# Optimization experiments

Hardware: AMD Instinct MI355X
Metric: run time of the kernel (lower is better)

## Reference

```python
import jax, jax.numpy as jnp
import numpy as np

OBS = jnp.array([0, 3, 6, 9, 12])
LO, HI = 0.001, 2.0

def gamma(x):
    return LO + (HI - LO) * jax.nn.sigmoid(x)

def full_chain_rhs(y, k):
    # y: (B,13) species, k: (B,19) rate constants
    A, B_, C, D, E, F, G, H, I, J, K_, L, M = [y[..., i] for i in range(13)]
    (kf1, kf2, kf3, kf4, kf5, kf6, kf7, kf8, kf9, kf10, kf11, kf12,
     kr1, kr3, kr5, kr7, kr9, kr11, kr12) = [k[..., i] for i in range(19)]
    dA = -kf1 * A + kr1 * B_
    dB = kf1 * A - kr1 * B_ - kf2 * B_
    dC = kf2 * B_ - kf3 * C + kr3 * D
    dD = kf3 * C - kr3 * D - kf4 * D
    dE = kf4 * D - kf5 * E + kr5 * F
    dF = kf5 * E - kr5 * F - kf6 * F
    dG = kf6 * F - kf7 * G + kr7 * H
    dH = kf7 * G - kr7 * H - kf8 * H
    dI = kf8 * H - kf9 * I + kr9 * J
    dJ = kf9 * I - kr9 * J - kf10 * J
    dK = kf10 * J - kf11 * K_ + kr11 * L
    dL = kf11 * K_ - kr11 * L - kf12 * L + kr12 * M
    dM = kf12 * L - kr12 * M
    return jnp.stack([dA, dB, dC, dD, dE, dF, dG, dH, dI, dJ, dK, dL, dM], axis=-1)

def rk4_step(y, dt, k):
    # y:(B,13) dt:(B,1) k:(B,19)
    k1 = full_chain_rhs(y, k)
    k2 = full_chain_rhs(y + 0.5 * dt * k1, k)
    k3 = full_chain_rhs(y + 0.5 * dt * k2, k)
    k4 = full_chain_rhs(y + dt * k3, k)
    return jnp.maximum(y + dt / 6.0 * (k1 + 2.0 * k2 + 2.0 * k3 + k4), 0.0)

def setup_inputs() -> dict:
    B, K, U, P = 2048, 256, 4, 5
    LIFT, HID = 32, 128
    key = jax.random.key(0)
    ks = jax.random.split(key, 9)
    in_dim = U + P
    def xavier(k, shape):
        lim = np.sqrt(6.0 / (shape[0] + shape[1])).astype(np.float32)
        return jax.random.uniform(k, shape, jnp.float32, -lim, lim)
    return {
        "y0": jax.random.uniform(ks[0], (B, P), jnp.float32),
        "u_seq": jax.random.normal(ks[1], (B, K, U), jnp.float32) * 0.1,
        "dt_seq": jax.random.uniform(ks[2], (B, K), jnp.float32, 0.01, 0.1),
        "y_seq": jax.random.uniform(ks[3], (B, K, P), jnp.float32),
        "W_lift": xavier(ks[4], (in_dim, LIFT)),
        "b_lift": jnp.zeros((LIFT,), jnp.float32),
        "w_ih": xavier(ks[5], (3 * HID, LIFT)),
        "w_hh": xavier(ks[6], (3 * HID, HID)),
        "b_ih": jnp.zeros((3 * HID,), jnp.float32),
        "b_hh": jnp.zeros((3 * HID,), jnp.float32),
        "W_head": xavier(ks[7], (HID, 19)),
        "b_head": jnp.zeros((19,), jnp.float32),
        "u_to_y_jump": jax.random.normal(ks[8], (U, P), jnp.float32) * 0.05,
        "tf_every": 50,
    }

def reference(y0, u_seq, dt_seq, y_seq, W_lift, b_lift, w_ih, w_hh, b_ih, b_hh, W_head, b_head, u_to_y_jump, tf_every):
    B, K, _ = u_seq.shape
    HID = w_hh.shape[1]
    # init hidden full state: 0.01 everywhere, obs slots get y0 + 0.01
    y_full0 = jnp.full((B, 13), 0.01, u_seq.dtype).at[:, OBS].set(y0 + 0.01)
    h0 = jnp.zeros((B, HID), u_seq.dtype)
    t = jnp.arange(K)
    tf_mask = (t > 0) & (t % tf_every == 0)  # teacher-forcing steps
    y_seq_prev = jnp.concatenate([jnp.zeros_like(y_seq[:, :1]), y_seq[:, :-1]], axis=1)
    xs = (jnp.swapaxes(u_seq, 0, 1), dt_seq.T[..., None],
          jnp.swapaxes(y_seq_prev, 0, 1), tf_mask)

    def step(carry, x):
        y_full, h = carry
        u_k, dt_k, y_prev_tf, m = x
        y_obs_prev = y_full[:, OBS]
        y_prev_in = jax.lax.stop_gradient(jnp.where(m, y_prev_tf, y_obs_prev))
        feat = jnp.concatenate([u_k, y_prev_in], axis=-1)
        lifted = jax.nn.silu(feat @ W_lift + b_lift)
        # PyTorch GRU cell
        gx = lifted @ w_ih.T + b_ih
        gh = h @ w_hh.T + b_hh
        rx, zx, nx = jnp.split(gx, 3, axis=-1)
        rh, zh, nh = jnp.split(gh, 3, axis=-1)
        r = jax.nn.sigmoid(rx + rh)
        z = jax.nn.sigmoid(zx + zh)
        n = jnp.tanh(nx + r * nh)
        h_new = (1.0 - z) * n + z * h
        theta = gamma(h_new @ W_head + b_head)  # (B,19), all bounds (0.001,2.0)
        y_obs_jump = y_obs_prev + u_k @ u_to_y_jump
        y_full_jump = y_full.at[:, OBS].set(y_obs_jump)
        y_full_next = rk4_step(y_full_jump, dt_k, theta)  # n_sub=1 as in forward
        return (y_full_next, h_new), (y_full_next[:, OBS], theta)

    _, (y_out, theta_out) = jax.lax.scan(step, (y_full0, h0), xs)
    return jnp.swapaxes(y_out, 0, 1), jnp.swapaxes(theta_out, 0, 1)
```

## Files before the change

### kernel.cpp

```cpp
#include <hip/hip_runtime.h>
#include <cstddef>
#include <cstdint>

#define NB 8
#define NTHREADS 640
#define HID 128
#define LIFT 32
#define NSP 13
#define NTH 19

typedef __attribute__((ext_vector_type(8))) short short8;
typedef __attribute__((ext_vector_type(4))) float f32x4;

__device__ const int c_kA [13] = {19,0,1,2,3,4,5,6,7,8,9,10,11};
__device__ const int c_kB1[13] = {0,12,2,13,4,14,6,15,8,16,10,17,18};
__device__ const int c_kB2[13] = {19,1,19,3,19,5,19,7,19,9,19,11,19};
__device__ const int c_kC [13] = {12,19,13,19,14,19,15,19,16,19,17,18,19};

__device__ __forceinline__ uint32_t pk(float a, float b) {
  uint32_t ua = __float_as_uint(a), ub = __float_as_uint(b);
  ua = (ua + 0x7FFFu + ((ua >> 16) & 1u)) >> 16;
  ub = (ub + 0x7FFFu + ((ub >> 16) & 1u)) >> 16;
  return ua | (ub << 16);
}
__device__ __forceinline__ float sigm(float a) { return 1.f/(1.f + __expf(-a)); }

__device__ __forceinline__ void sync_lds() {
  __builtin_amdgcn_sched_barrier(0);
  asm volatile("s_waitcnt lgkmcnt(0)" ::: "memory");
  __builtin_amdgcn_s_barrier();
  __builtin_amdgcn_sched_barrier(0);
}

__device__ __forceinline__ float rhs3(int am1, int ap1, float cA, float cB,
                                      float cC, float yc) {
  const float ym1 = __int_as_float(__builtin_amdgcn_ds_bpermute(am1, __float_as_int(yc)));
  const float yp1 = __int_as_float(__builtin_amdgcn_ds_bpermute(ap1, __float_as_int(yc)));
  return fmaf(cA, ym1, fmaf(cB, yc, cC * yp1));
}

union FragU { uint4 u; short8 s; };
__device__ __forceinline__ short8 ldfrag(const float* p) {
  FragU t;
  const float4 a = *reinterpret_cast<const float4*>(p);
  const float4 b = *reinterpret_cast<const float4*>(p+4);
  t.u = make_uint4(pk(a.x,a.y), pk(a.z,a.w), pk(b.x,b.y), pk(b.z,b.w));
  return t.s;
}

struct Smem {
  uint32_t whF[8*3*4*64*4];
  uint32_t whdF[2*4*64*4];
  uint32_t hF[4*64*4];
  uint32_t liftF[64*4];
  float theta[8*20];
};

__global__ __launch_bounds__(NTHREADS)
void fullmodel_rnn(const float* __restrict__ y0,
                   const float* __restrict__ u_seq,
                   const float* __restrict__ dt_seq,
                   const float* __restrict__ y_seq,
                   const float* __restrict__ W_lift,
                   const float* __restrict__ b_lift,
                   const float* __restrict__ w_ih,
                   const float* __restrict__ w_hh,
                   const float* __restrict__ b_ih,
                   const float* __restrict__ b_hh,
                   const float* __restrict__ W_head,
                   const float* __restrict__ b_head,
                   const float* __restrict__ u2y,
                   const int*  __restrict__ tf_every_p,
                   float* __restrict__ out,
                   int K, int theta_off)
{
  extern __shared__ __align__(16) char smem_raw[];
  Smem& S = *reinterpret_cast<Smem*>(smem_raw);

  const int tid  = threadIdx.x;
  const int wid  = tid >> 6;
  const int lane = tid & 63;
  const int q    = lane >> 4;
  const int col  = lane & 15;
  const int bg0  = blockIdx.x * NB;
  const int tf_every = tf_every_p[0];
  const bool gatew = (wid < 8);

  for (int f = tid; f < 8*3*4*64; f += NTHREADS) {
    int l = f & 63, idx = f >> 6;
    int s = idx & 3; idx >>= 2;
    int g = idx % 3, w = idx / 3;
    int row = 128*g + 16*w + (l & 15);
    int k0 = 32*s + 8*(l >> 4);
    const float* p = w_hh + (size_t)row*HID + k0;
    uint32_t* d = S.whF + (size_t)f*4;
    d[0]=pk(p[0],p[1]); d[1]=pk(p[2],p[3]); d[2]=pk(p[4],p[5]); d[3]=pk(p[6],p[7]);
  }
  for (int f = tid; f < 2*4*64; f += NTHREADS) {
    int l = f & 63, idx = f >> 6;
    int s = idx & 3, T = idx >> 2;
    int o = 16*T + (l & 15);
    int k0 = 32*s + 8*(l >> 4);
    uint32_t* d = S.whdF + (size_t)f*4;
    if (o < NTH) {
#pragma unroll
      for (int c=0;c<4;++c)
        d[c] = pk(W_head[(size_t)(k0+2*c)*NTH + o], W_head[(size_t)(k0+2*c+1)*NTH + o]);
    } else {
#pragma unroll
      for (int c=0;c<4;++c) d[c] = 0u;
    }
  }
  for (int f = tid; f < 4*64*4; f += NTHREADS) S.hF[f] = 0u;
  for (int f = tid; f < 64*4;   f += NTHREADS) S.liftF[f] = 0u;
  if (tid < 8) S.theta[tid*20 + 19] = 0.f;

  const uint32_t* hf_p  = &S.hF[lane*4];
  const uint32_t* lf_p  = &S.liftF[lane*4];
  const uint32_t* whp   = S.whF + ((size_t)wid*12*64 + lane)*4;
  const uint32_t* whdp  = S.whdF + (size_t)lane*4;

  float bsumR[4], bsumZ[4], bihn_[4], bhhn_[4], h_old[4];
  short8 wir, wiz, win;
  if (gatew) {
    const int rowR = 16*wid + col, kq = 8*q;
    wir = ldfrag(w_ih + (size_t)rowR*LIFT + kq);
    wiz = ldfrag(w_ih + (size_t)(128+rowR)*LIFT + kq);
    win = ldfrag(w_ih + (size_t)(256+rowR)*LIFT + kq);
#pragma unroll
    for (int r2=0;r2<4;++r2) {
      const int i0 = 16*wid + 4*q + r2;
      bsumR[r2] = b_ih[i0]     + b_hh[i0];
      bsumZ[r2] = b_ih[128+i0] + b_hh[128+i0];
      bihn_[r2] = b_ih[256+i0];
      bhhn_[r2] = b_hh[256+i0];
      h_old[r2] = 0.f;
    }
  }

  float bhd[2][4] = {{0,0,0,0},{0,0,0,0}};
  float wa0=0,wa1=0,wa2=0,wa3=0,wa4=0,wa5=0,wa6=0,wa7=0,wa8=0;
  float wb0=0,wb1=0,wb2=0,wb3=0,wb4=0,wb5=0,wb6=0,wb7=0,wb8=0;
  float blA=0.f, blB=0.f;
  const int base_b = (wid == 9) ? 4 : 0;
  const int b_loc = lane / NSP, rs = lane - NSP*b_loc;
  const bool rk_lane = (!gatew) && (lane < 52);
  const int bl8 = base_b + b_loc;
  const int gb = bg0 + (rk_lane ? bl8 : 0);
  const int gbL = bg0 + base_b + (lane >> 4);
  const bool obs = rk_lane && (rs % 3 == 0);
  const int ro = rs / 3;
  float y_reg=0.f, f_src=0.f;
  float u2yv[4]={0,0,0,0};
  int kA_=0,kB1_=0,kB2_=0,kC_=0;
  int am1=0, ap1=0, tfc=1;
  float dt_c=0.f, ysq_c=0.f;
  float4 ujc = {0,0,0,0};
  float* outT0 = out; float* outY = out;
  if (!gatew) {
#pragma unroll
    for (int T=0;T<2;++T)
#pragma unroll
      for (int r2=0;r2<4;++r2) {
        const int o = 16*T + 4*q + r2;
        bhd[T][r2] = (o < NTH) ? b_head[o] : 0.f;
      }
    const int li = 2*col;
    wa0=W_lift[0*32+li]; wa1=W_lift[1*32+li]; wa2=W_lift[2*32+li];
    wa3=W_lift[3*32+li]; wa4=W_lift[4*32+li]; wa5=W_lift[5*32+li];
    wa6=W_lift[6*32+li]; wa7=W_lift[7*32+li]; wa8=W_lift[8*32+li];
    wb0=W_lift[0*32+li+1]; wb1=W_lift[1*32+li+1]; wb2=W_lift[2*32+li+1];
    wb3=W_lift[3*32+li+1]; wb4=W_lift[4*32+li+1]; wb5=W_lift[5*32+li+1];
    wb6=W_lift[6*32+li+1]; wb7=W_lift[7*32+li+1]; wb8=W_lift[8*32+li+1];
    blA = b_lift[li]; blB = b_lift[li+1];
    outT0 = out + (size_t)theta_off + ((size_t)(bg0+col))*K*NTH + 4*q;
    __builtin_amdgcn_s_setprio(2);
  }
  if (rk_lane) {
    kA_ = c_kA[rs]; kB1_ = c_kB1[rs]; kB2_ = c_kB2[rs]; kC_ = c_kC[rs];
    am1 = 4 * ((lane > 0)  ? (lane - 1) : 0);
    ap1 = 4 * ((lane < 51) ? (lane + 1) : 51);
    y_reg = 0.01f + (obs ? y0[gb*5 + ro] : 0.f);
    if (obs) { for (int d=0;d<4;++d) u2yv[d] = u2y[d*5 + ro]; }
    f_src = y_reg;
    outY = out + ((size_t)gb*K)*5 + ro;
  }
  sync_lds();

  for (int k = 0; k <= K; ++k) {
    f32x4 accR={0,0,0,0}, accZ={0,0,0,0}, accNH={0,0,0,0};

    if (gatew) {
      if (k < K) {
        FragU h0,h1,h2,h3;
        h0.u = *reinterpret_cast<const uint4*>(hf_p);
        h1.u = *reinterpret_cast<const uint4*>(hf_p + 256);
        h2.u = *reinterpret_cast<const uint4*>(hf_p + 512);
        h3.u = *reinterpret_cast<const uint4*>(hf_p + 768);
#pragma unroll
        for (int ss=0; ss<4; ++ss) {
          FragU ar,az,an;
          ar.u = *reinterpret_cast<const uint4*>(whp + (0*4+ss)*256);
          az.u = *reinterpret_cast<const uint4*>(whp + (1*4+ss)*256);
          an.u = *reinterpret_cast<const uint4*>(whp + (2*4+ss)*256);
          const short8 hb = (ss==0)?h0.s:(ss==1)?h1.s:(ss==2)?h2.s:h3.s;
          accR  = __builtin_amdgcn_mfma_f32_16x16x32_bf16(ar.s, hb, accR, 0,0,0);
          accZ  = __builtin_amdgcn_mfma_f32_16x16x32_bf16(az.s, hb, accZ, 0,0,0);
          accNH = __builtin_amdgcn_mfma_f32_16x16x32_bf16(an.s, hb, accNH, 0,0,0);
        }
      }
    } else {
      float dt_p=0.f, ysq_p=0.f;
      float4 ujp = {0,0,0,0}, ul = {0,0,0,0};
      if (k < K) {
        if (rk_lane) {
          dt_p = dt_seq[(size_t)gb*K + k];
          ujp  = *reinterpret_cast<const float4*>(u_seq + ((size_t)gb*K + k)*4);
          if (obs) ysq_p = y_seq[((size_t)gb*K + k)*5 + ro];
        }
        ul = *reinterpret_cast<const float4*>(u_seq + ((size_t)gbL*K + k)*4);
      }
      if (k >= 1) {
        f32x4 at0={0,0,0,0}, at1={0,0,0,0};
        FragU h0,h1,h2,h3;
        h0.u = *reinterpret_cast<const uint4*>(hf_p);
        h1.u = *reinterpret_cast<const uint4*>(hf_p + 256);
        h2.u = *reinterpret_cast<const uint4*>(hf_p + 512);
        h3.u = *reinterpret_cast<const uint4*>(hf_p + 768);
#pragma unroll
        for (int ss=0; ss<4; ++ss) {
          FragU a0,a1;
          a0.u = *reinterpret_cast<const uint4*>(whdp + (0*4+ss)*256);
          a1.u = *reinterpret_cast<const uint4*>(whdp + (1*4+ss)*256);
          const short8 hb = (ss==0)?h0.s:(ss==1)?h1.s:(ss==2)?h2.s:h3.s;
          at0 = __builtin_amdgcn_mfma_f32_16x16x32_bf16(a0.s, hb, at0, 0,0,0);
          at1 = __builtin_amdgcn_mfma_f32_16x16x32_bf16(a1.s, hb, at1, 0,0,0);
        }
        if (col >= base_b && col < base_b + 4) {
          f32x4 th0;
#pragma unroll
          for (int r2=0;r2<4;++r2) th0[r2] = 0.001f + 1.999f*sigm(at0[r2] + bhd[0][r2]);
          *reinterpret_cast<f32x4*>(&S.theta[col*20 + 4*q]) = th0;
          outT0[0]=th0[0]; outT0[1]=th0[1]; outT0[2]=th0[2]; outT0[3]=th0[3];
          if (q == 0) {
            f32x4 th1;
#pragma unroll
            for (int r2=0;r2<4;++r2) th1[r2] = 0.001f + 1.999f*sigm(at1[r2] + bhd[1][r2]);
            outT0[16]=th1[0]; outT0[17]=th1[1]; outT0[18]=th1[2];
            th1[3] = 0.f;
            *reinterpret_cast<f32x4*>(&S.theta[col*20 + 16]) = th1;
          }
        }
        if (rk_lane) {
          const float dtv = dt_c;
          const float* thp = S.theta + bl8*20;
          const float cA = thp[kA_];
          const float cB = -(thp[kB1_] + thp[kB2_]);
          const float cC = thp[kC_];
          float yj = y_reg;
          if (obs) yj += ujc.x*u2yv[0] + ujc.y*u2yv[1] + ujc.z*u2yv[2] + ujc.w*u2yv[3];
          float yc = yj;
          const float k1 = rhs3(am1, ap1, cA, cB, cC, yc);
          yc = fmaf(0.5f*dtv, k1, yj);
          const float k2 = rhs3(am1, ap1, cA, cB, cC, yc);
          yc = fmaf(0.5f*dtv, k2, yj);
          const float k3 = rhs3(am1, ap1, cA, cB, cC, yc);
          yc = fmaf(dtv, k3, yj);
          const float k4 = rhs3(am1, ap1, cA, cB, cC, yc);
          const float yn = fmaxf(fmaf(dtv*(1.f/6.f), k1 + 2.f*k2 + 2.f*k3 + k4, yj), 0.f);
          y_reg = yn;
          if (obs) *outY = yn;
          if (k < K) {
            const bool m_next = (tfc == tf_every);
            tfc = m_next ? 1 : (tfc + 1);
            if (obs) f_src = m_next ? ysq_c : yn;
          }
        }
        outT0 += NTH; outY += 5;
      }
      if (k < K) {
        const int g4 = NSP*(lane >> 4);
        const float fy0 = __shfl(f_src, g4+0), fy1 = __shfl(f_src, g4+3);
        const float fy2 = __shfl(f_src, g4+6), fy3 = __shfl(f_src, g4+9);
        const float fy4 = __shfl(f_src, g4+12);
        float a = blA + ul.x*wa0 + ul.y*wa1 + ul.z*wa2 + ul.w*wa3
                      + fy0*wa4 + fy1*wa5 + fy2*wa6 + fy3*wa7 + fy4*wa8;
        float b = blB + ul.x*wb0 + ul.y*wb1 + ul.z*wb2 + ul.w*wb3
                      + fy0*wb4 + fy1*wb5 + fy2*wb6 + fy3*wb7 + fy4*wb8;
        const float va = a*sigm(a), vb = b*sigm(b);
        const int bL = base_b + (lane >> 4);
        S.liftF[(col>>2)*64 + bL*4 + (col&3)] = pk(va, vb);
      }
      dt_c = dt_p; ysq_c = ysq_p; ujc = ujp;
    }
    sync_lds();

    if (gatew && k < K) {
      FragU lf; lf.u = *reinterpret_cast<const uint4*>(lf_p);
      accR = __builtin_amdgcn_mfma_f32_16x16x32_bf16(wir, lf.s, accR, 0,0,0);
      accZ = __builtin_amdgcn_mfma_f32_16x16x32_bf16(wiz, lf.s, accZ, 0,0,0);
      f32x4 z4 = {0,0,0,0};
      f32x4 accNX = __builtin_amdgcn_mfma_f32_16x16x32_bf16(win, lf.s, z4, 0,0,0);
      float hn[4];
#pragma unroll
      for (int r2=0;r2<4;++r2) {
        const float rg = sigm(accR[r2] + bsumR[r2]);
        const float zg = sigm(accZ[r2] + bsumZ[r2]);
        const float nx = accNX[r2] + bihn_[r2];
        const float nh = accNH[r2] + bhhn_[r2];
        const float e  = __expf(2.f*(nx + rg*nh));
        const float ng = 1.f - 2.f/(e + 1.f);
        hn[r2] = (1.f - zg)*ng + zg*h_old[r2];
        h_old[r2] = hn[r2];
      }
      const int word = (wid>>1)*256 + ((((2*wid)+(q>>1))&3)*16 + col)*4 + 2*(q&1);
      *reinterpret_cast<uint2*>(&S.hF[word]) = make_uint2(pk(hn[0],hn[1]), pk(hn[2],hn[3]));
    }
    sync_lds();
  }
}

extern "C" void kernel_launch(void* const* d_in, const int* in_sizes, int n_in,
                              void* d_out, int out_size, void* d_ws, size_t ws_size,
                              hipStream_t stream) {
  const float* y0     = (const float*)d_in[0];
  const float* u_seq  = (const float*)d_in[1];
  const float* dt_seq = (const float*)d_in[2];
  const float* y_seq  = (const float*)d_in[3];
  const float* W_lift = (const float*)d_in[4];
  const float* b_lift = (const float*)d_in[5];
  const float* w_ih   = (const float*)d_in[6];
  const float* w_hh   = (const float*)d_in[7];
  const float* b_ih   = (const float*)d_in[8];
  const float* b_hh   = (const float*)d_in[9];
  const float* W_head = (const float*)d_in[10];
  const float* b_head = (const float*)d_in[11];
  const float* u2y    = (const float*)d_in[12];
  const int*   tfe    = (const int*)d_in[13];
  float* out = (float*)d_out;

  const int B = in_sizes[0] / 5;
  const int K = in_sizes[2] / B;
  const int theta_off = B * K * 5;

  (void)hipFuncSetAttribute((const void*)fullmodel_rnn,
                            hipFuncAttributeMaxDynamicSharedMemorySize,
                            (int)sizeof(Smem));

  dim3 grid(B / NB), block(NTHREADS);
  hipLaunchKernelGGL(fullmodel_rnn, grid, block, sizeof(Smem), stream,
                     y0, u_seq, dt_seq, y_seq, W_lift, b_lift, w_ih, w_hh,
                     b_ih, b_hh, W_head, b_head, u2y, tfe, out, K, theta_off);
}
```

Before: 647.1 us.

## Keep recurrent and head weight fragments in registers instead of LDS

```diff
diff --git a/kernel.cpp b/kernel.cpp
--- a/kernel.cpp
+++ b/kernel.cpp
@@ -49,14 +49,13 @@
 }
 
 struct Smem {
-  uint32_t whF[8*3*4*64*4];
-  uint32_t whdF[2*4*64*4];
   uint32_t hF[4*64*4];
   uint32_t liftF[64*4];
   float theta[8*20];
 };
 
-__global__ __launch_bounds__(NTHREADS)
+__global__ __attribute__((amdgpu_flat_work_group_size(NTHREADS, NTHREADS),
+                          amdgpu_waves_per_eu(2)))
 void fullmodel_rnn(const float* __restrict__ y0,
                    const float* __restrict__ u_seq,
                    const float* __restrict__ dt_seq,
@@ -74,8 +73,7 @@
                    float* __restrict__ out,
                    int K, int theta_off)
 {
-  extern __shared__ __align__(16) char smem_raw[];
-  Smem& S = *reinterpret_cast<Smem*>(smem_raw);
+  __shared__ Smem S;
 
   const int tid  = threadIdx.x;
   const int wid  = tid >> 6;
@@ -86,39 +84,14 @@
   const int tf_every = tf_every_p[0];
   const bool gatew = (wid < 8);
 
-  for (int f = tid; f < 8*3*4*64; f += NTHREADS) {
-    int l = f & 63, idx = f >> 6;
-    int s = idx & 3; idx >>= 2;
-    int g = idx % 3, w = idx / 3;
-    int row = 128*g + 16*w + (l & 15);
-    int k0 = 32*s + 8*(l >> 4);
-    const float* p = w_hh + (size_t)row*HID + k0;
-    uint32_t* d = S.whF + (size_t)f*4;
-    d[0]=pk(p[0],p[1]); d[1]=pk(p[2],p[3]); d[2]=pk(p[4],p[5]); d[3]=pk(p[6],p[7]);
-  }
-  for (int f = tid; f < 2*4*64; f += NTHREADS) {
-    int l = f & 63, idx = f >> 6;
-    int s = idx & 3, T = idx >> 2;
-    int o = 16*T + (l & 15);
-    int k0 = 32*s + 8*(l >> 4);
-    uint32_t* d = S.whdF + (size_t)f*4;
-    if (o < NTH) {
-#pragma unroll
-      for (int c=0;c<4;++c)
-        d[c] = pk(W_head[(size_t)(k0+2*c)*NTH + o], W_head[(size_t)(k0+2*c+1)*NTH + o]);
-    } else {
-#pragma unroll
-      for (int c=0;c<4;++c) d[c] = 0u;
-    }
-  }
   for (int f = tid; f < 4*64*4; f += NTHREADS) S.hF[f] = 0u;
   for (int f = tid; f < 64*4;   f += NTHREADS) S.liftF[f] = 0u;
   if (tid < 8) S.theta[tid*20 + 19] = 0.f;
 
   const uint32_t* hf_p  = &S.hF[lane*4];
   const uint32_t* lf_p  = &S.liftF[lane*4];
-  const uint32_t* whp   = S.whF + ((size_t)wid*12*64 + lane)*4;
-  const uint32_t* whdp  = S.whdF + (size_t)lane*4;
+
+  short8 afrag[12];
 
   float bsumR[4], bsumZ[4], bihn_[4], bhhn_[4], h_old[4];
   short8 wir, wiz, win;
@@ -127,6 +100,13 @@
     wir = ldfrag(w_ih + (size_t)rowR*LIFT + kq);
     wiz = ldfrag(w_ih + (size_t)(128+rowR)*LIFT + kq);
     win = ldfrag(w_ih + (size_t)(256+rowR)*LIFT + kq);
+    const float* wb = w_hh + (size_t)rowR*HID + kq;
+#pragma unroll
+    for (int ss=0; ss<4; ++ss) {
+      afrag[ss]   = ldfrag(wb + 32*ss);
+      afrag[4+ss] = ldfrag(wb + (size_t)128*HID + 32*ss);
+      afrag[8+ss] = ldfrag(wb + (size_t)256*HID + 32*ss);
+    }
 #pragma unroll
     for (int r2=0;r2<4;++r2) {
       const int i0 = 16*wid + 4*q + r2;
@@ -158,6 +138,23 @@
   float4 ujc = {0,0,0,0};
   float* outT0 = out; float* outY = out;
   if (!gatew) {
+#pragma unroll
+    for (int T=0; T<2; ++T)
+#pragma unroll
+      for (int ss=0; ss<4; ++ss) {
+        const int o  = 16*T + col;
+        const int k0 = 32*ss + 8*q;
+        FragU t;
+        if (o < NTH) {
+          t.u.x = pk(W_head[(size_t)(k0+0)*NTH + o], W_head[(size_t)(k0+1)*NTH + o]);
+          t.u.y = pk(W_head[(size_t)(k0+2)*NTH + o], W_head[(size_t)(k0+3)*NTH + o]);
+          t.u.z = pk(W_head[(size_t)(k0+4)*NTH + o], W_head[(size_t)(k0+5)*NTH + o]);
+          t.u.w = pk(W_head[(size_t)(k0+6)*NTH + o], W_head[(size_t)(k0+7)*NTH + o]);
+        } else {
+          t.u = make_uint4(0u,0u,0u,0u);
+        }
+        afrag[T*4+ss] = t.s;
+      }
 #pragma unroll
     for (int T=0;T<2;++T)
 #pragma unroll
@@ -199,14 +196,10 @@
         h3.u = *reinterpret_cast<const uint4*>(hf_p + 768);
 #pragma unroll
         for (int ss=0; ss<4; ++ss) {
-          FragU ar,az,an;
-          ar.u = *reinterpret_cast<const uint4*>(whp + (0*4+ss)*256);
-          az.u = *reinterpret_cast<const uint4*>(whp + (1*4+ss)*256);
-          an.u = *reinterpret_cast<const uint4*>(whp + (2*4+ss)*256);
           const short8 hb = (ss==0)?h0.s:(ss==1)?h1.s:(ss==2)?h2.s:h3.s;
-          accR  = __builtin_amdgcn_mfma_f32_16x16x32_bf16(ar.s, hb, accR, 0,0,0);
-          accZ  = __builtin_amdgcn_mfma_f32_16x16x32_bf16(az.s, hb, accZ, 0,0,0);
-          accNH = __builtin_amdgcn_mfma_f32_16x16x32_bf16(an.s, hb, accNH, 0,0,0);
+          accR  = __builtin_amdgcn_mfma_f32_16x16x32_bf16(afrag[ss],   hb, accR, 0,0,0);
+          accZ  = __builtin_amdgcn_mfma_f32_16x16x32_bf16(afrag[4+ss], hb, accZ, 0,0,0);
+          accNH = __builtin_amdgcn_mfma_f32_16x16x32_bf16(afrag[8+ss], hb, accNH, 0,0,0);
         }
       }
     } else {
@@ -229,12 +222,9 @@
         h3.u = *reinterpret_cast<const uint4*>(hf_p + 768);
 #pragma unroll
         for (int ss=0; ss<4; ++ss) {
-          FragU a0,a1;
-          a0.u = *reinterpret_cast<const uint4*>(whdp + (0*4+ss)*256);
-          a1.u = *reinterpret_cast<const uint4*>(whdp + (1*4+ss)*256);
           const short8 hb = (ss==0)?h0.s:(ss==1)?h1.s:(ss==2)?h2.s:h3.s;
-          at0 = __builtin_amdgcn_mfma_f32_16x16x32_bf16(a0.s, hb, at0, 0,0,0);
-          at1 = __builtin_amdgcn_mfma_f32_16x16x32_bf16(a1.s, hb, at1, 0,0,0);
+          at0 = __builtin_amdgcn_mfma_f32_16x16x32_bf16(afrag[ss],   hb, at0, 0,0,0);
+          at1 = __builtin_amdgcn_mfma_f32_16x16x32_bf16(afrag[4+ss], hb, at1, 0,0,0);
         }
         if (col >= base_b && col < base_b + 4) {
           f32x4 th0;
@@ -343,12 +333,8 @@
   const int K = in_sizes[2] / B;
   const int theta_off = B * K * 5;
 
-  (void)hipFuncSetAttribute((const void*)fullmodel_rnn,
-                            hipFuncAttributeMaxDynamicSharedMemorySize,
-                            (int)sizeof(Smem));
-
   dim3 grid(B / NB), block(NTHREADS);
-  hipLaunchKernelGGL(fullmodel_rnn, grid, block, sizeof(Smem), stream,
+  hipLaunchKernelGGL(fullmodel_rnn, grid, block, 0, stream,
                      y0, u_seq, dt_seq, y_seq, W_lift, b_lift, w_ih, w_hh,
                      b_ih, b_hh, W_head, b_head, u2y, tfe, out, K, theta_off);
 }
```

Measured after the change: 674.6 us. +4.2%, slower.

## Halve batch per block and stream packed w_hh fragments from global memory

Applied to the files above, without the earlier changes.

```diff
diff --git a/kernel.cpp b/kernel.cpp
--- a/kernel.cpp
+++ b/kernel.cpp
@@ -2,12 +2,13 @@
 #include <cstddef>
 #include <cstdint>
 
-#define NB 8
-#define NTHREADS 640
+#define NB 4
+#define NTHREADS 576
 #define HID 128
 #define LIFT 32
 #define NSP 13
 #define NTH 19
+
 
 typedef __attribute__((ext_vector_type(8))) short short8;
 typedef __attribute__((ext_vector_type(4))) float f32x4;
@@ -49,12 +50,25 @@
 }
 
 struct Smem {
-  uint32_t whF[8*3*4*64*4];
   uint32_t whdF[2*4*64*4];
   uint32_t hF[4*64*4];
   uint32_t liftF[64*4];
-  float theta[8*20];
+  float theta[4*20];
 };
+
+__global__ __launch_bounds__(256)
+void prep_whf(const float* __restrict__ w_hh, uint4* __restrict__ ws) {
+  const int f = blockIdx.x*256 + threadIdx.x;
+  if (f >= 8*3*4*64) return;
+  const int l = f & 63;
+  int idx = f >> 6;
+  const int s = idx & 3; idx >>= 2;
+  const int g = idx % 3, w = idx / 3;
+  const int row = 128*g + 16*w + (l & 15);
+  const int k0  = 32*s + 8*(l >> 4);
+  const float* p = w_hh + (size_t)row*HID + k0;
+  ws[f] = make_uint4(pk(p[0],p[1]), pk(p[2],p[3]), pk(p[4],p[5]), pk(p[6],p[7]));
+}
 
 __global__ __launch_bounds__(NTHREADS)
 void fullmodel_rnn(const float* __restrict__ y0,
@@ -64,18 +78,17 @@
                    const float* __restrict__ W_lift,
                    const float* __restrict__ b_lift,
                    const float* __restrict__ w_ih,
-                   const float* __restrict__ w_hh,
                    const float* __restrict__ b_ih,
                    const float* __restrict__ b_hh,
                    const float* __restrict__ W_head,
                    const float* __restrict__ b_head,
                    const float* __restrict__ u2y,
                    const int*  __restrict__ tf_every_p,
+                   const uint4* __restrict__ whf,
                    float* __restrict__ out,
                    int K, int theta_off)
 {
-  extern __shared__ __align__(16) char smem_raw[];
-  Smem& S = *reinterpret_cast<Smem*>(smem_raw);
+  __shared__ Smem S;
 
   const int tid  = threadIdx.x;
   const int wid  = tid >> 6;
@@ -86,16 +99,6 @@
   const int tf_every = tf_every_p[0];
   const bool gatew = (wid < 8);
 
-  for (int f = tid; f < 8*3*4*64; f += NTHREADS) {
-    int l = f & 63, idx = f >> 6;
-    int s = idx & 3; idx >>= 2;
-    int g = idx % 3, w = idx / 3;
-    int row = 128*g + 16*w + (l & 15);
-    int k0 = 32*s + 8*(l >> 4);
-    const float* p = w_hh + (size_t)row*HID + k0;
-    uint32_t* d = S.whF + (size_t)f*4;
-    d[0]=pk(p[0],p[1]); d[1]=pk(p[2],p[3]); d[2]=pk(p[4],p[5]); d[3]=pk(p[6],p[7]);
-  }
   for (int f = tid; f < 2*4*64; f += NTHREADS) {
     int l = f & 63, idx = f >> 6;
     int s = idx & 3, T = idx >> 2;
@@ -113,12 +116,12 @@
   }
   for (int f = tid; f < 4*64*4; f += NTHREADS) S.hF[f] = 0u;
   for (int f = tid; f < 64*4;   f += NTHREADS) S.liftF[f] = 0u;
-  if (tid < 8) S.theta[tid*20 + 19] = 0.f;
+  if (tid < 4) S.theta[tid*20 + 19] = 0.f;
 
   const uint32_t* hf_p  = &S.hF[lane*4];
   const uint32_t* lf_p  = &S.liftF[lane*4];
-  const uint32_t* whp   = S.whF + ((size_t)wid*12*64 + lane)*4;
   const uint32_t* whdp  = S.whdF + (size_t)lane*4;
+  const uint4*    whp   = whf + (size_t)wid*12*64 + lane;
 
   float bsumR[4], bsumZ[4], bihn_[4], bhhn_[4], h_old[4];
   short8 wir, wiz, win;
@@ -142,12 +145,10 @@
   float wa0=0,wa1=0,wa2=0,wa3=0,wa4=0,wa5=0,wa6=0,wa7=0,wa8=0;
   float wb0=0,wb1=0,wb2=0,wb3=0,wb4=0,wb5=0,wb6=0,wb7=0,wb8=0;
   float blA=0.f, blB=0.f;
-  const int base_b = (wid == 9) ? 4 : 0;
   const int b_loc = lane / NSP, rs = lane - NSP*b_loc;
   const bool rk_lane = (!gatew) && (lane < 52);
-  const int bl8 = base_b + b_loc;
-  const int gb = bg0 + (rk_lane ? bl8 : 0);
-  const int gbL = bg0 + base_b + (lane >> 4);
+  const int gb = bg0 + (rk_lane ? b_loc : 0);
+  const int gbL = bg0 + (lane >> 4);
   const bool obs = rk_lane && (rs % 3 == 0);
   const int ro = rs / 3;
   float y_reg=0.f, f_src=0.f;
@@ -200,9 +201,9 @@
 #pragma unroll
         for (int ss=0; ss<4; ++ss) {
           FragU ar,az,an;
-          ar.u = *reinterpret_cast<const uint4*>(whp + (0*4+ss)*256);
-          az.u = *reinterpret_cast<const uint4*>(whp + (1*4+ss)*256);
-          an.u = *reinterpret_cast<const uint4*>(whp + (2*4+ss)*256);
+          ar.u = whp[(0*4+ss)*64];
+          az.u = whp[(1*4+ss)*64];
+          an.u = whp[(2*4+ss)*64];
           const short8 hb = (ss==0)?h0.s:(ss==1)?h1.s:(ss==2)?h2.s:h3.s;
           accR  = __builtin_amdgcn_mfma_f32_16x16x32_bf16(ar.s, hb, accR, 0,0,0);
           accZ  = __builtin_amdgcn_mfma_f32_16x16x32_bf16(az.s, hb, accZ, 0,0,0);
@@ -236,7 +237,7 @@
           at0 = __builtin_amdgcn_mfma_f32_16x16x32_bf16(a0.s, hb, at0, 0,0,0);
           at1 = __builtin_amdgcn_mfma_f32_16x16x32_bf16(a1.s, hb, at1, 0,0,0);
         }
-        if (col >= base_b && col < base_b + 4) {
+        if (col < 4) {
           f32x4 th0;
 #pragma unroll
           for (int r2=0;r2<4;++r2) th0[r2] = 0.001f + 1.999f*sigm(at0[r2] + bhd[0][r2]);
@@ -253,7 +254,7 @@
         }
         if (rk_lane) {
           const float dtv = dt_c;
-          const float* thp = S.theta + bl8*20;
+          const float* thp = S.theta + b_loc*20;
           const float cA = thp[kA_];
           const float cB = -(thp[kB1_] + thp[kB2_]);
           const float cC = thp[kC_];
@@ -288,7 +289,7 @@
         float b = blB + ul.x*wb0 + ul.y*wb1 + ul.z*wb2 + ul.w*wb3
                       + fy0*wb4 + fy1*wb5 + fy2*wb6 + fy3*wb7 + fy4*wb8;
         const float va = a*sigm(a), vb = b*sigm(b);
-        const int bL = base_b + (lane >> 4);
+        const int bL = lane >> 4;
         S.liftF[(col>>2)*64 + bL*4 + (col&3)] = pk(va, vb);
       }
       dt_c = dt_p; ysq_c = ysq_p; ujc = ujp;
@@ -343,12 +344,13 @@
   const int K = in_sizes[2] / B;
   const int theta_off = B * K * 5;
 
-  (void)hipFuncSetAttribute((const void*)fullmodel_rnn,
-                            hipFuncAttributeMaxDynamicSharedMemorySize,
-                            (int)sizeof(Smem));
+  uint4* whf = (uint4*)d_ws;
+
+  hipLaunchKernelGGL(prep_whf, dim3((8*3*4*64 + 255)/256), dim3(256), 0, stream,
+                     w_hh, whf);
 
   dim3 grid(B / NB), block(NTHREADS);
-  hipLaunchKernelGGL(fullmodel_rnn, grid, block, sizeof(Smem), stream,
-                     y0, u_seq, dt_seq, y_seq, W_lift, b_lift, w_ih, w_hh,
-                     b_ih, b_hh, W_head, b_head, u2y, tfe, out, K, theta_off);
-}
+  hipLaunchKernelGGL(fullmodel_rnn, grid, block, 0, stream,
+                     y0, u_seq, dt_seq, y_seq, W_lift, b_lift, w_ih,
+                     b_ih, b_hh, W_head, b_head, u2y, tfe, whf, out, K, theta_off);
+}
```

Measured after the change: 1.240 ms. 1.92x slower.

## Rewrite RK4 step as Taylor series with pentadiagonal operator, move lift weights to LDS

Applied to the files above, without the earlier changes.

```diff
diff --git a/kernel.cpp b/kernel.cpp
--- a/kernel.cpp
+++ b/kernel.cpp
@@ -12,10 +12,15 @@
 typedef __attribute__((ext_vector_type(8))) short short8;
 typedef __attribute__((ext_vector_type(4))) float f32x4;
 
-__device__ const int c_kA [13] = {19,0,1,2,3,4,5,6,7,8,9,10,11};
-__device__ const int c_kB1[13] = {0,12,2,13,4,14,6,15,8,16,10,17,18};
-__device__ const int c_kB2[13] = {19,1,19,3,19,5,19,7,19,9,19,11,19};
-__device__ const int c_kC [13] = {12,19,13,19,14,19,15,19,16,19,17,18,19};
+#define PKI(a,b,c,d) ((uint32_t)(a)|((uint32_t)(b)<<5)|((uint32_t)(c)<<10)|((uint32_t)(d)<<15))
+__device__ const uint32_t c_pk2[15] = {
+  PKI(19,19,19,19),
+  PKI(19, 0,19,12), PKI( 0,12, 1,19), PKI( 1, 2,19,13), PKI( 2,13, 3,19),
+  PKI( 3, 4,19,14), PKI( 4,14, 5,19), PKI( 5, 6,19,15), PKI( 6,15, 7,19),
+  PKI( 7, 8,19,16), PKI( 8,16, 9,19), PKI( 9,10,19,17), PKI(10,17,11,18),
+  PKI(11,18,19,19),
+  PKI(19,19,19,19)
+};
 
 __device__ __forceinline__ uint32_t pk(float a, float b) {
   uint32_t ua = __float_as_uint(a), ub = __float_as_uint(b);
@@ -24,19 +29,15 @@
   return ua | (ub << 16);
 }
 __device__ __forceinline__ float sigm(float a) { return 1.f/(1.f + __expf(-a)); }
+__device__ __forceinline__ float bperm(int addr, float v) {
+  return __int_as_float(__builtin_amdgcn_ds_bpermute(addr, __float_as_int(v)));
+}
 
 __device__ __forceinline__ void sync_lds() {
   __builtin_amdgcn_sched_barrier(0);
   asm volatile("s_waitcnt lgkmcnt(0)" ::: "memory");
   __builtin_amdgcn_s_barrier();
   __builtin_amdgcn_sched_barrier(0);
-}
-
-__device__ __forceinline__ float rhs3(int am1, int ap1, float cA, float cB,
-                                      float cC, float yc) {
-  const float ym1 = __int_as_float(__builtin_amdgcn_ds_bpermute(am1, __float_as_int(yc)));
-  const float yp1 = __int_as_float(__builtin_amdgcn_ds_bpermute(ap1, __float_as_int(yc)));
-  return fmaf(cA, ym1, fmaf(cB, yc, cC * yp1));
 }
 
 union FragU { uint4 u; short8 s; };
@@ -54,6 +55,8 @@
   uint32_t hF[4*64*4];
   uint32_t liftF[64*4];
   float theta[8*20];
+  float bh[20];
+  float2 wl[10*16];
 };
 
 __global__ __launch_bounds__(NTHREADS)
@@ -113,7 +116,15 @@
   }
   for (int f = tid; f < 4*64*4; f += NTHREADS) S.hF[f] = 0u;
   for (int f = tid; f < 64*4;   f += NTHREADS) S.liftF[f] = 0u;
-  if (tid < 8) S.theta[tid*20 + 19] = 0.f;
+  if (tid < 8)  S.theta[tid*20 + 19] = 0.f;
+  if (tid < 20) S.bh[tid] = (tid < NTH) ? b_head[tid] : 0.f;
+  if (tid < 160) {
+    const int r = tid >> 4, c = tid & 15;
+    float2 w;
+    if (r < 9) { w.x = W_lift[r*32 + 2*c]; w.y = W_lift[r*32 + 2*c + 1]; }
+    else       { w.x = b_lift[2*c];        w.y = b_lift[2*c + 1]; }
+    S.wl[tid] = w;
+  }
 
   const uint32_t* hf_p  = &S.hF[lane*4];
   const uint32_t* lf_p  = &S.liftF[lane*4];
@@ -138,10 +149,6 @@
     }
   }
 
-  float bhd[2][4] = {{0,0,0,0},{0,0,0,0}};
-  float wa0=0,wa1=0,wa2=0,wa3=0,wa4=0,wa5=0,wa6=0,wa7=0,wa8=0;
-  float wb0=0,wb1=0,wb2=0,wb3=0,wb4=0,wb5=0,wb6=0,wb7=0,wb8=0;
-  float blA=0.f, blB=0.f;
   const int base_b = (wid == 9) ? 4 : 0;
   const int b_loc = lane / NSP, rs = lane - NSP*b_loc;
   const bool rk_lane = (!gatew) && (lane < 52);
@@ -152,34 +159,21 @@
   const int ro = rs / 3;
   float y_reg=0.f, f_src=0.f;
   float u2yv[4]={0,0,0,0};
-  int kA_=0,kB1_=0,kB2_=0,kC_=0;
-  int am1=0, ap1=0, tfc=1;
+  uint32_t pm=0, p0=0, pp=0;
+  int am1=0, ap1=0, am2=0, ap2=0, tfc=1;
   float dt_c=0.f, ysq_c=0.f;
   float4 ujc = {0,0,0,0};
   float* outT0 = out; float* outY = out;
   if (!gatew) {
-#pragma unroll
-    for (int T=0;T<2;++T)
-#pragma unroll
-      for (int r2=0;r2<4;++r2) {
-        const int o = 16*T + 4*q + r2;
-        bhd[T][r2] = (o < NTH) ? b_head[o] : 0.f;
-      }
-    const int li = 2*col;
-    wa0=W_lift[0*32+li]; wa1=W_lift[1*32+li]; wa2=W_lift[2*32+li];
-    wa3=W_lift[3*32+li]; wa4=W_lift[4*32+li]; wa5=W_lift[5*32+li];
-    wa6=W_lift[6*32+li]; wa7=W_lift[7*32+li]; wa8=W_lift[8*32+li];
-    wb0=W_lift[0*32+li+1]; wb1=W_lift[1*32+li+1]; wb2=W_lift[2*32+li+1];
-    wb3=W_lift[3*32+li+1]; wb4=W_lift[4*32+li+1]; wb5=W_lift[5*32+li+1];
-    wb6=W_lift[6*32+li+1]; wb7=W_lift[7*32+li+1]; wb8=W_lift[8*32+li+1];
-    blA = b_lift[li]; blB = b_lift[li+1];
     outT0 = out + (size_t)theta_off + ((size_t)(bg0+col))*K*NTH + 4*q;
     __builtin_amdgcn_s_setprio(2);
   }
   if (rk_lane) {
-    kA_ = c_kA[rs]; kB1_ = c_kB1[rs]; kB2_ = c_kB2[rs]; kC_ = c_kC[rs];
-    am1 = 4 * ((lane > 0)  ? (lane - 1) : 0);
-    ap1 = 4 * ((lane < 51) ? (lane + 1) : 51);
+    pm = c_pk2[rs]; p0 = c_pk2[rs+1]; pp = c_pk2[rs+2];
+    am1 = 4 * ((lane >= 1)  ? (lane - 1) : 0);
+    am2 = 4 * ((lane >= 2)  ? (lane - 2) : 0);
+    ap1 = 4 * ((lane <= 50) ? (lane + 1) : 51);
+    ap2 = 4 * ((lane <= 49) ? (lane + 2) : 51);
     y_reg = 0.01f + (obs ? y0[gb*5 + ro] : 0.f);
     if (obs) { for (int d=0;d<4;++d) u2yv[d] = u2y[d*5 + ro]; }
     f_src = y_reg;
@@ -221,6 +215,13 @@
         ul = *reinterpret_cast<const float4*>(u_seq + ((size_t)gbL*K + k)*4);
       }
       if (k >= 1) {
+        float yj=0.f, y_m1=0.f, y_p1=0.f, y_m2=0.f, y_p2=0.f;
+        if (rk_lane) {
+          yj = y_reg;
+          if (obs) yj += ujc.x*u2yv[0] + ujc.y*u2yv[1] + ujc.z*u2yv[2] + ujc.w*u2yv[3];
+          y_m1 = bperm(am1, yj); y_p1 = bperm(ap1, yj);
+          y_m2 = bperm(am2, yj); y_p2 = bperm(ap2, yj);
+        }
         f32x4 at0={0,0,0,0}, at1={0,0,0,0};
         FragU h0,h1,h2,h3;
         h0.u = *reinterpret_cast<const uint4*>(hf_p);
@@ -237,15 +238,17 @@
           at1 = __builtin_amdgcn_mfma_f32_16x16x32_bf16(a1.s, hb, at1, 0,0,0);
         }
         if (col >= base_b && col < base_b + 4) {
+          const f32x4 bh0 = *reinterpret_cast<const f32x4*>(&S.bh[4*q]);
           f32x4 th0;
 #pragma unroll
-          for (int r2=0;r2<4;++r2) th0[r2] = 0.001f + 1.999f*sigm(at0[r2] + bhd[0][r2]);
+          for (int r2=0;r2<4;++r2) th0[r2] = 0.001f + 1.999f*sigm(at0[r2] + bh0[r2]);
           *reinterpret_cast<f32x4*>(&S.theta[col*20 + 4*q]) = th0;
           outT0[0]=th0[0]; outT0[1]=th0[1]; outT0[2]=th0[2]; outT0[3]=th0[3];
           if (q == 0) {
+            const f32x4 bh1 = *reinterpret_cast<const f32x4*>(&S.bh[16]);
             f32x4 th1;
 #pragma unroll
-            for (int r2=0;r2<4;++r2) th1[r2] = 0.001f + 1.999f*sigm(at1[r2] + bhd[1][r2]);
+            for (int r2=0;r2<4;++r2) th1[r2] = 0.001f + 1.999f*sigm(at1[r2] + bh1[r2]);
             outT0[16]=th1[0]; outT0[17]=th1[1]; outT0[18]=th1[2];
             th1[3] = 0.f;
             *reinterpret_cast<f32x4*>(&S.theta[col*20 + 16]) = th1;
@@ -253,21 +256,33 @@
         }
         if (rk_lane) {
           const float dtv = dt_c;
-          const float* thp = S.theta + bl8*20;
-          const float cA = thp[kA_];
-          const float cB = -(thp[kB1_] + thp[kB2_]);
-          const float cC = thp[kC_];
-          float yj = y_reg;
-          if (obs) yj += ujc.x*u2yv[0] + ujc.y*u2yv[1] + ujc.z*u2yv[2] + ujc.w*u2yv[3];
-          float yc = yj;
-          const float k1 = rhs3(am1, ap1, cA, cB, cC, yc);
-          yc = fmaf(0.5f*dtv, k1, yj);
-          const float k2 = rhs3(am1, ap1, cA, cB, cC, yc);
-          yc = fmaf(0.5f*dtv, k2, yj);
-          const float k3 = rhs3(am1, ap1, cA, cB, cC, yc);
-          yc = fmaf(dtv, k3, yj);
-          const float k4 = rhs3(am1, ap1, cA, cB, cC, yc);
-          const float yn = fmaxf(fmaf(dtv*(1.f/6.f), k1 + 2.f*k2 + 2.f*k3 + k4, yj), 0.f);
+          const float* thb = S.theta + bl8*20;
+          const float a_m = thb[pm & 31];
+          const float b_m = -(thb[(pm>>5) & 31] + thb[(pm>>10) & 31]);
+          const float c_m = thb[(pm>>15) & 31];
+          const float a0  = thb[p0 & 31];
+          const float b0  = -(thb[(p0>>5) & 31] + thb[(p0>>10) & 31]);
+          const float c0  = thb[(p0>>15) & 31];
+          const float a_p = thb[pp & 31];
+          const float b_p = -(thb[(pp>>5) & 31] + thb[(pp>>10) & 31]);
+          const float c_p = thb[(pp>>15) & 31];
+          const float r2m2 = a0*a_m;
+          const float r2m1 = a0*b_m + b0*a0;
+          const float r2c  = a0*c_m + b0*b0 + c0*a_p;
+          const float r2p1 = b0*c0 + c0*b_p;
+          const float r2p2 = c0*c_p;
+          const float s1 = a0*y_m1 + b0*yj + c0*y_p1;
+          const float z2 = r2m2*y_m2 + r2m1*y_m1 + r2c*yj + r2p1*y_p1 + r2p2*y_p2;
+          const float z_m1 = bperm(am1, z2), z_p1 = bperm(ap1, z2);
+          const float z_m2 = bperm(am2, z2), z_p2 = bperm(ap2, z2);
+          const float s3 = a0*z_m1 + b0*z2 + c0*z_p1;
+          const float s4 = r2m2*z_m2 + r2m1*z_m1 + r2c*z2 + r2p1*z_p1 + r2p2*z_p2;
+          const float dt2 = dtv*dtv;
+          float acc = fmaf(dtv, s1, yj);
+          acc = fmaf(dt2*0.5f, z2, acc);
+          acc = fmaf(dt2*dtv*(1.f/6.f), s3, acc);
+          acc = fmaf(dt2*dt2*(1.f/24.f), s4, acc);
+          const float yn = fmaxf(acc, 0.f);
           y_reg = yn;
           if (obs) *outY = yn;
           if (k < K) {
@@ -280,13 +295,17 @@
       }
       if (k < K) {
         const int g4 = NSP*(lane >> 4);
+        const float2 w0 = S.wl[0*16+col], w1 = S.wl[1*16+col], w2 = S.wl[2*16+col];
+        const float2 w3 = S.wl[3*16+col], w4 = S.wl[4*16+col], w5 = S.wl[5*16+col];
+        const float2 w6 = S.wl[6*16+col], w7 = S.wl[7*16+col], w8 = S.wl[8*16+col];
+        const float2 w9 = S.wl[9*16+col];
         const float fy0 = __shfl(f_src, g4+0), fy1 = __shfl(f_src, g4+3);
         const float fy2 = __shfl(f_src, g4+6), fy3 = __shfl(f_src, g4+9);
         const float fy4 = __shfl(f_src, g4+12);
-        float a = blA + ul.x*wa0 + ul.y*wa1 + ul.z*wa2 + ul.w*wa3
-                      + fy0*wa4 + fy1*wa5 + fy2*wa6 + fy3*wa7 + fy4*wa8;
-        float b = blB + ul.x*wb0 + ul.y*wb1 + ul.z*wb2 + ul.w*wb3
-                      + fy0*wb4 + fy1*wb5 + fy2*wb6 + fy3*wb7 + fy4*wb8;
+        float a = w9.x + ul.x*w0.x + ul.y*w1.x + ul.z*w2.x + ul.w*w3.x
+                       + fy0*w4.x + fy1*w5.x + fy2*w6.x + fy3*w7.x + fy4*w8.x;
+        float b = w9.y + ul.x*w0.y + ul.y*w1.y + ul.z*w2.y + ul.w*w3.y
+                       + fy0*w4.y + fy1*w5.y + fy2*w6.y + fy3*w7.y + fy4*w8.y;
         const float va = a*sigm(a), vb = b*sigm(b);
         const int bL = base_b + (lane >> 4);
         S.liftF[(col>>2)*64 + bL*4 + (col&3)] = pk(va, vb);
```

Result: slower. 682.6 us (+5.5%).
